# Kernel optimization log

Measured on AMD Instinct MI355X. Metric: run time of the kernel, lower is better.

Reference implementation:

```python
import jax, jax.numpy as jnp
import numpy as np
import math

B, S, D, H = 2, 2048, 4096, 32
HD = D // H  # head_dim = 128


def setup_inputs() -> dict:
    key = jax.random.key(0)
    ks = jax.random.split(key, 8)
    scale = 1.0 / math.sqrt(D)
    x = jax.random.normal(ks[0], (B, S, D), jnp.float32)
    wq = jax.random.normal(ks[1], (D, D), jnp.float32) * scale
    wk = jax.random.normal(ks[2], (D, D), jnp.float32) * scale
    wv = jax.random.normal(ks[3], (D, D), jnp.float32) * scale
    wo = jax.random.normal(ks[4], (D, D), jnp.float32) * scale
    # vis_adapter_gate is zero-initialized in the module; use small random to exercise the path
    wg = jax.random.normal(ks[5], (H, D), jnp.float32) * 0.02
    # RoPE angles: theta[t, i] = t / 10000^(2i/HD), shape (S, HD//2)
    inv_freq = 1.0 / (10000.0 ** (jnp.arange(0, HD, 2, dtype=jnp.float32) / HD))
    freqs = jnp.arange(S, dtype=jnp.float32)[:, None] * inv_freq[None, :]
    # additive causal mask (1,1,S,S)
    neg = jnp.float32(-1e9)
    mask = jnp.where(jnp.tril(jnp.ones((S, S), bool)), 0.0, neg)[None, None]
    image_position = jax.random.bernoulli(ks[6], 0.3, (B, S, D))
    return {"x": x, "wq": wq, "wk": wk, "wv": wv, "wo": wo, "wg": wg,
            "freqs": freqs, "mask": mask, "image_position": image_position}


def _rope(t, cos, sin):
    # t: (B,S,H,HD), cos/sin: (1,S,1,HD//2). Pairs are consecutive elements.
    t2 = t.reshape(*t.shape[:-1], HD // 2, 2)
    tr, ti = t2[..., 0], t2[..., 1]
    out = jnp.stack([tr * cos - ti * sin, tr * sin + ti * cos], axis=-1)
    return out.reshape(t.shape)


def reference(x, wq, wk, wv, wo, wg, freqs, mask, image_position):
    xq = jnp.einsum('bsd,ed->bse', x, wq).reshape(B, S, H, HD)
    xk = jnp.einsum('bsd,ed->bse', x, wk).reshape(B, S, H, HD)
    xv = jnp.einsum('bsd,ed->bse', x, wv).reshape(B, S, H, HD)
    # value gating on image positions
    xg = jnp.tanh(jnp.einsum('bsd,hd->bsh', x, wg))[..., None]  # (B,S,H,1)
    ip = image_position.reshape(B, S, H, HD)
    xv = jnp.where(ip, xv * xg, xv)
    # rotary embedding (computed in float32 as in torch .float())
    cos = jnp.cos(freqs)[None, :, None, :]
    sin = jnp.sin(freqs)[None, :, None, :]
    xq = _rope(xq, cos, sin)
    xk = _rope(xk, cos, sin)
    # (B,H,S,HD)
    q = xq.transpose(0, 2, 1, 3)
    k = xk.transpose(0, 2, 1, 3)
    v = xv.transpose(0, 2, 1, 3)
    scores = jnp.einsum('bhqd,bhkd->bhqk', q, k) / math.sqrt(HD) + mask
    probs = jax.nn.softmax(scores.astype(jnp.float32), axis=-1).astype(q.dtype)
    out = jnp.einsum('bhqk,bhkd->bhqd', probs, v)
    out = out.transpose(0, 2, 1, 3).reshape(B, S, D)
    return jnp.einsum('bsd,ed->bse', out, wo)
```

## Files before the change

kernel.cpp:

```cpp
#include <hip/hip_runtime.h>
#include <hip/hip_bf16.h>
#include <stdint.h>

#define B_ 2
#define S_ 2048
#define D_ 4096
#define H_ 32
#define HD_ 128
#define MTOK (B_*S_)
#define QK_SCALE 0.08838834764831845f

typedef __attribute__((ext_vector_type(8))) __bf16 bf8;
typedef __attribute__((ext_vector_type(4))) float f32x4;
typedef __attribute__((ext_vector_type(4))) unsigned short us4;
typedef __attribute__((ext_vector_type(8))) unsigned short us8;
typedef unsigned short u16;
typedef __attribute__((address_space(1))) unsigned gu32;
typedef __attribute__((address_space(3))) unsigned lu32;

__device__ __forceinline__ u16 f2bf(float f){
  unsigned u = __builtin_bit_cast(unsigned, f);
  u += 0x7FFFu + ((u >> 16) & 1u);
  return (u16)(u >> 16);
}
__device__ __forceinline__ float bf2f(u16 h){
  unsigned u = ((unsigned)h) << 16;
  return __builtin_bit_cast(float, u);
}
__device__ __forceinline__ void gload16(const void* g, void* l){
  __builtin_amdgcn_global_load_lds((gu32*)g, (lu32*)l, 16, 0, 0);
}
__device__ __forceinline__ f32x4 mfma_bf16(bf8 a, bf8 b, f32x4 c){
  return __builtin_amdgcn_mfma_f32_16x16x32_bf16(a, b, c, 0, 0, 0);
}
__device__ __forceinline__ bool read_ip(const void* p, int flag, size_t idx){
  if (flag == 0) return ((const int*)p)[idx] != 0;
  if (flag == 1) return ((const unsigned char*)p)[idx] != 0;
  if (flag == 2) return ((const u16*)p)[idx] != 0;
  return ((const float*)p)[idx] != 0.0f;
}

__global__ void k_detect(const void* x, const void* ip, const void* fq, int* flags){
  const int lane = threadIdx.x & 63;
  const unsigned char* xb = (const unsigned char*)x;
  int cnt = 0;
  for (int i = lane; i < 256; i += 64){
    unsigned char b = xb[i*4 + 1] & 0x7F;
    if (b >= 0x3A && b <= 0x41) cnt++;
  }
  #pragma unroll
  for (int off = 1; off < 64; off <<= 1) cnt += __shfl_xor(cnt, off);
  const int fflag = (cnt >= 128) ? 1 : 0;

  const unsigned char* q = (const unsigned char*)ip;
  int nz1 = 0, nz2 = 0, nz3 = 0, mx = 0;
  for (int i = lane; i < 4096; i += 64){
    int v = q[i];
    if (v > mx) mx = v;
    if (v){ int m = i & 3; if (m == 1) nz1 = 1; else if (m == 2) nz2 = 1; else if (m == 3) nz3 = 1; }
  }
  nz1 = __any(nz1); nz2 = __any(nz2); nz3 = __any(nz3);
  #pragma unroll
  for (int off = 1; off < 64; off <<= 1) mx = max(mx, __shfl_xor(mx, off));
  int ipflag;
  if (!nz1 && !nz2 && !nz3) ipflag = 0;
  else if (mx <= 1)         ipflag = 1;
  else if (nz1)             ipflag = 2;
  else                      ipflag = 3;

  const unsigned char* fb = (const unsigned char*)fq;
  int nzf = 0;
  for (int i = 128 + lane; i < 256; i += 64) if (fb[i]) nzf = 1;
  nzf = __any(nzf);
  if (lane == 0){ flags[0] = ipflag; flags[1] = fflag; flags[2] = nzf; }
}

struct CArgs {
  const float* src[6];
  u16* dst[6];
  int n4[6];
};
__global__ void k_convert_all(CArgs a, const int* __restrict__ flags){
  if (flags[1]) return;
  int pre[7];
  pre[0] = 0;
  #pragma unroll
  for (int s = 0; s < 6; ++s) pre[s+1] = pre[s] + a.n4[s];
  const int total = pre[6];
  int i = blockIdx.x * blockDim.x + threadIdx.x;
  const int stride = gridDim.x * blockDim.x;
  for (; i < total; i += stride){
    int s = 0;
    #pragma unroll
    for (int k = 1; k < 6; ++k) if (i >= pre[k]) s = k;
    const int j = i - pre[s];
    float4 v = ((const float4*)a.src[s])[j];
    us4 o;
    o.x = f2bf(v.x); o.y = f2bf(v.y); o.z = f2bf(v.z); o.w = f2bf(v.w);
    ((us4*)a.dst[s])[j] = o;
  }
}

__global__ void k_trig(const void* freqs, float* ctab, float* stab, const int* flags){
  int i = blockIdx.x * blockDim.x + threadIdx.x;
  if (i >= S_ * (HD_/2)) return;
  float v = flags[2] ? bf2f(((const u16*)freqs)[i]) : ((const float*)freqs)[i];
  ctab[i] = cosf(v);
  stab[i] = sinf(v);
}

__global__ __launch_bounds__(256,2) void k_gate(const void* x_raw, const u16* x_conv,
                                                const void* wg_raw, const u16* wg_conv,
                                                float* G, const int* flags){
  const int fflag = flags[1];
  const u16* X  = fflag ? (const u16*)x_raw  : x_conv;
  const u16* WG = fflag ? (const u16*)wg_raw : wg_conv;
  const int t = threadIdx.x, lane = t & 63, wid = t >> 6;
  const int hi = lane >> 4, lo = lane & 15, sw = lane & 7;
  const int m0 = (int)blockIdx.x * 64;
  __shared__ __align__(16) u16 lX[64*64];
  __shared__ __align__(16) u16 lW[32*64];
  f32x4 acc[2] = {};
  for (int kt = 0; kt < D_/64; ++kt){
    __syncthreads();
    const int kb = kt * 64;
    #pragma unroll
    for (int qi = 0; qi < 2; ++qi){
      int ci = t + qi*256;
      int row = ci >> 3, sc = (ci & 7) ^ (row & 7);
      gload16(X + (size_t)(m0 + row)*D_ + kb + sc*8, &lX[ci*8]);
    }
    {
      int ci = t;
      if (ci < 256){
        int row = ci >> 3, sc = (ci & 7) ^ (row & 7);
        gload16(WG + (size_t)row*D_ + kb + sc*8, &lW[ci*8]);
      }
    }
    __syncthreads();
    #pragma unroll
    for (int kk = 0; kk < 2; ++kk){
      bf8 a = *(const bf8*)&lX[(wid*16 + lo)*64 + (((kk*4 + hi) ^ sw)*8)];
      #pragma unroll
      for (int n = 0; n < 2; ++n){
        bf8 b = *(const bf8*)&lW[(n*16 + lo)*64 + (((kk*4 + hi) ^ sw)*8)];
        acc[n] = mfma_bf16(a, b, acc[n]);
      }
    }
  }
  #pragma unroll
  for (int n = 0; n < 2; ++n)
    #pragma unroll
    for (int r = 0; r < 4; ++r){
      const int tok = m0 + wid*16 + (hi << 2) + r;
      const int h = n*16 + lo;
      G[(size_t)tok*H_ + h] = tanhf(acc[n][r]);
    }
}

struct GArgs {
  const void* a_raw; const u16* a_conv;
  const void* w_raw0; const u16* w_conv0;
  const void* w_raw1; const u16* w_conv1;
  const void* w_raw2; const u16* w_conv2;
  const int* flags;
  const float* ctab; const float* stab; const float* G;
  const void* ip;
  u16* Qs; u16* Ks; u16* VT;
  void* out;
  int mode;
};

__global__ __launch_bounds__(256,2) void k_gemm(GArgs g){
  const int t = threadIdx.x;
  const int fflag = g.flags[1];
  int mat, nt;
  if (g.mode < 0){ mat = (int)blockIdx.y >> 5; nt = (int)blockIdx.y & 31; }
  else           { mat = 3; nt = (int)blockIdx.y; }
  const int wi = (mat == 3) ? 0 : mat;
  const void* wraw; const u16* wconv;
  if (wi == 0){ wraw = g.w_raw0; wconv = g.w_conv0; }
  else if (wi == 1){ wraw = g.w_raw1; wconv = g.w_conv1; }
  else { wraw = g.w_raw2; wconv = g.w_conv2; }
  const u16* Ap = fflag ? (const u16*)g.a_raw : g.a_conv;
  const u16* Wp = fflag ? (const u16*)wraw : wconv;
  const int m0 = (int)blockIdx.x * 128;
  const int n0 = nt * 128;
  __shared__ __align__(16) u16 lA[128*64];
  __shared__ __align__(16) u16 lB[128*64];
  const int lane = t & 63, wid = t >> 6;
  const int wrw = wid >> 1, wcw = wid & 1;
  const int hi = lane >> 4, lo = lane & 15, sw = lane & 7;
  f32x4 acc[4][4] = {};
  for (int kt = 0; kt < D_/64; ++kt){
    __syncthreads();
    const int kb = kt * 64;
    #pragma unroll
    for (int qi = 0; qi < 4; ++qi){
      int ci = t + qi*256;
      int row = ci >> 3, sc = (ci & 7) ^ (row & 7);
      gload16(Ap + (size_t)(m0 + row)*D_ + kb + sc*8, &lA[ci*8]);
    }
    #pragma unroll
    for (int qi = 0; qi < 4; ++qi){
      int ci = t + qi*256;
      int row = ci >> 3, sc = (ci & 7) ^ (row & 7);
      gload16(Wp + (size_t)(n0 + row)*D_ + kb + sc*8, &lB[ci*8]);
    }
    __syncthreads();
    #pragma unroll
    for (int kk = 0; kk < 2; ++kk){
      bf8 af[4], bfr[4];
      #pragma unroll
      for (int m = 0; m < 4; ++m)
        af[m] = *(const bf8*)&lA[(wrw*64 + m*16 + lo)*64 + (((kk*4 + hi) ^ sw)*8)];
      #pragma unroll
      for (int n = 0; n < 4; ++n)
        bfr[n] = *(const bf8*)&lB[(wcw*64 + n*16 + lo)*64 + (((kk*4 + hi) ^ sw)*8)];
      #pragma unroll
      for (int m = 0; m < 4; ++m)
        #pragma unroll
        for (int n = 0; n < 4; ++n)
          acc[m][n] = mfma_bf16(af[m], bfr[n], acc[m][n]);
    }
  }
  const int rbase = m0 + wrw*64 + (hi << 2);
  const int cbase = n0 + wcw*64 + lo;
  if (mat == 0 || mat == 1){
    u16* dst = (mat == 0) ? g.Qs : g.Ks;
    const float sc = (mat == 0) ? QK_SCALE : 1.0f;
    #pragma unroll
    for (int m = 0; m < 4; ++m){
      #pragma unroll
      for (int n = 0; n < 4; ++n){
        const int e = cbase + n*16;
        const int h = e >> 7, hd = e & 127, pr = hd >> 1;
        const bool even = ((hd & 1) == 0);
        #pragma unroll
        for (int r = 0; r < 4; ++r){
          const int row = rbase + m*16 + r;
          const int b = row >> 11, s = row & (S_-1);
          float v = acc[m][n][r];
          float o = __shfl_xor(v, 1);
          float cc = g.ctab[s*64 + pr], sn = g.stab[s*64 + pr];
          float res = even ? (v*cc - o*sn) : (o*sn + v*cc);
          res *= sc;
          dst[((size_t)(b*H_ + h)*S_ + s)*HD_ + hd] = f2bf(res);
        }
      }
    }
  } else if (mat == 2){
    const int ipf = g.flags[0];
    #pragma unroll
    for (int m = 0; m < 4; ++m){
      const int row0 = rbase + m*16;
      const int b = row0 >> 11, s0 = row0 & (S_-1);
      #pragma unroll
      for (int n = 0; n < 4; ++n){
        const int e = cbase + n*16;
        const int h = e >> 7, hd = e & 127;
        us4 pk;
        #pragma unroll
        for (int r = 0; r < 4; ++r){
          const int s = s0 + r;
          float v = acc[m][n][r];
          size_t ii = (size_t)(b*S_ + s)*D_ + e;
          if (read_ip(g.ip, ipf, ii)) v *= g.G[(size_t)(b*S_ + s)*H_ + h];
          pk[r] = f2bf(v);
        }
        *(us4*)&g.VT[((size_t)(b*H_ + h)*HD_ + hd)*S_ + s0] = pk;
      }
    }
  } else {
    #pragma unroll
    for (int m = 0; m < 4; ++m){
      #pragma unroll
      for (int n = 0; n < 4; ++n){
        const int e = cbase + n*16;
        #pragma unroll
        for (int r = 0; r < 4; ++r){
          const int row = rbase + m*16 + r;
          float v = acc[m][n][r];
          if (fflag) ((u16*)g.out)[(size_t)row*D_ + e] = f2bf(v);
          else       ((float*)g.out)[(size_t)row*D_ + e] = v;
        }
      }
    }
  }
}

__global__ __launch_bounds__(256,2) void k_attn(const u16* __restrict__ Qs, const u16* __restrict__ Ks,
                                                const u16* __restrict__ VT, u16* __restrict__ AO){
  const int bh = blockIdx.x;
  const int qb = (int)(gridDim.y - 1 - blockIdx.y) * 128;
  const u16* Qp = Qs + (size_t)bh * S_ * HD_;
  const u16* Kp = Ks + (size_t)bh * S_ * HD_;
  const u16* Vp = VT + (size_t)bh * HD_ * S_;
  const int t = threadIdx.x, lane = t & 63, w = t >> 6;
  const int q0 = qb + w*32;
  const int hi = lane >> 4, lo = lane & 15, sw = lane & 7;
  __shared__ __align__(16) u16 lK[2][64*HD_];
  __shared__ __align__(16) u16 lV[2][HD_*64];
  __shared__ __align__(16) u16 lP[4][32*64];

  const us8 ones_u = {0x3F80,0x3F80,0x3F80,0x3F80,0x3F80,0x3F80,0x3F80,0x3F80};
  const bf8 ones = __builtin_bit_cast(bf8, ones_u);

  auto stage = [&](int j2, int bsel){
    const int kv = j2 * 64;
    #pragma unroll
    for (int qi = 0; qi < 4; ++qi){
      int ci = t + qi*256;
      int row = ci >> 4, scs = (ci & 15) ^ (row & 7);
      gload16(Kp + (size_t)(kv + row)*HD_ + scs*8, &lK[bsel][ci*8]);
    }
    #pragma unroll
    for (int qi = 0; qi < 4; ++qi){
      int ci = t + qi*256;
      int row = ci >> 3, scs = (ci & 7) ^ (row & 7);
      gload16(Vp + (size_t)row*S_ + kv + scs*8, &lV[bsel][ci*8]);
    }
  };

  bf8 qf[2][4];
  #pragma unroll
  for (int m = 0; m < 2; ++m)
    #pragma unroll
    for (int kk = 0; kk < 4; ++kk)
      qf[m][kk] = *(const bf8*)&Qp[(size_t)(q0 + m*16 + lo)*HD_ + kk*32 + hi*8];
  f32x4 o[2][8] = {};
  f32x4 osum[2] = {};
  const int ntile = (qb >> 6) + 2;

  stage(0, 0);
  stage(1, 1);
  asm volatile("s_waitcnt vmcnt(8)" ::: "memory");
  __builtin_amdgcn_s_barrier();

  for (int j = 0; j < ntile; ++j){
    const int cur = j & 1;
    const int kv0 = j*64;
    if (kv0 <= q0 + 31){
      f32x4 sf[2][4] = {};
      __builtin_amdgcn_s_setprio(1);
      #pragma unroll
      for (int kk = 0; kk < 4; ++kk){
        bf8 kf[4];
        #pragma unroll
        for (int n = 0; n < 4; ++n)
          kf[n] = *(const bf8*)&lK[cur][(n*16 + lo)*HD_ + (((kk*4 + hi) ^ sw)*8)];
        #pragma unroll
        for (int m = 0; m < 2; ++m)
          #pragma unroll
          for (int n = 0; n < 4; ++n)
            sf[m][n] = mfma_bf16(qf[m][kk], kf[n], sf[m][n]);
      }
      __builtin_amdgcn_s_setprio(0);
      const int rb = q0 + (hi << 2);
      const int cb = kv0 + lo;
      #pragma unroll
      for (int m = 0; m < 2; ++m)
        #pragma unroll
        for (int r = 0; r < 4; ++r){
          const int row = rb + m*16 + r;
          #pragma unroll
          for (int n = 0; n < 4; ++n){
            float s = (cb + n*16 > row) ? -1e30f : sf[m][n][r];
            sf[m][n][r] = __expf(fminf(s, 80.0f));
          }
        }
      u16* myP = lP[w];
      #pragma unroll
      for (int m = 0; m < 2; ++m)
        #pragma unroll
        for (int n = 0; n < 4; ++n)
          #pragma unroll
          for (int r = 0; r < 4; ++r){
            const int prow = m*16 + (hi << 2) + r;
            myP[prow*64 + ((n*16 + lo) ^ ((prow & 7) << 3))] = f2bf(sf[m][n][r]);
          }
      __builtin_amdgcn_s_setprio(1);
      #pragma unroll
      for (int kk = 0; kk < 2; ++kk){
        bf8 pf[2];
        #pragma unroll
        for (int m = 0; m < 2; ++m)
          pf[m] = *(const bf8*)&myP[(m*16 + lo)*64 + ((kk*32 + hi*8) ^ (sw << 3))];
        #pragma unroll
        for (int n = 0; n < 8; ++n){
          bf8 vf = *(const bf8*)&lV[cur][(n*16 + lo)*64 + (((kk*4 + hi) ^ sw)*8)];
          #pragma unroll
          for (int m = 0; m < 2; ++m)
            o[m][n] = mfma_bf16(pf[m], vf, o[m][n]);
        }
        #pragma unroll
        for (int m = 0; m < 2; ++m)
          osum[m] = mfma_bf16(pf[m], ones, osum[m]);
      }
      __builtin_amdgcn_s_setprio(0);
    }
    __builtin_amdgcn_s_barrier();
    if (j + 2 < ntile){
      stage(j + 2, cur);
      asm volatile("s_waitcnt vmcnt(8)" ::: "memory");
    } else if (j + 1 < ntile){
      asm volatile("s_waitcnt vmcnt(0)" ::: "memory");
    }
    __builtin_amdgcn_s_barrier();
  }
  const int b = bh >> 5, h = bh & 31;
  #pragma unroll
  for (int m = 0; m < 2; ++m){
    #pragma unroll
    for (int n = 0; n < 8; ++n){
      const int c = n*16 + lo;
      #pragma unroll
      for (int r = 0; r < 4; ++r){
        const int row = q0 + m*16 + (hi << 2) + r;
        float v = o[m][n][r] / osum[m][r];
        AO[(size_t)(b*S_ + row)*D_ + h*HD_ + c] = f2bf(v);
      }
    }
  }
}

extern "C" void kernel_launch(void* const* d_in, const int* in_sizes, int n_in,
                              void* d_out, int out_size, void* d_ws, size_t ws_size,
                              hipStream_t stream){
  const void* x   = d_in[0];
  const void* wq  = d_in[1];
  const void* wk  = d_in[2];
  const void* wv  = d_in[3];
  const void* wo  = d_in[4];
  const void* wg  = d_in[5];
  const void* fr  = d_in[6];
  const void* ip  = d_in[8];

  char* ws = (char*)d_ws;
  size_t off = 0;
  auto alloc = [&](size_t bytes)->char* {
    size_t o = off; off += (bytes + 255) & ~(size_t)255; return ws + o;
  };
  int*   flags = (int*)  alloc(256);
  float* ctab  = (float*)alloc((size_t)S_*64*4);
  float* stab  = (float*)alloc((size_t)S_*64*4);
  float* G     = (float*)alloc((size_t)MTOK*H_*4);
  u16* Qs = (u16*)alloc((size_t)B_*H_*S_*HD_*2);
  u16* Ks = (u16*)alloc((size_t)B_*H_*S_*HD_*2);
  u16* VT = (u16*)alloc((size_t)B_*H_*S_*HD_*2);
  u16* AO = (u16*)alloc((size_t)MTOK*D_*2);
  size_t conv_bytes = ((size_t)MTOK*D_*2 + 256) + 4*((size_t)D_*D_*2 + 256) + ((size_t)H_*D_*2 + 256);
  bool conv = (ws_size >= off + conv_bytes);
  u16 *xb = Qs, *wqb = Qs, *wkb = Qs, *wvb = Qs, *wob = Qs, *wgb = Qs;
  if (conv){
    xb  = (u16*)alloc((size_t)MTOK*D_*2);
    wqb = (u16*)alloc((size_t)D_*D_*2);
    wkb = (u16*)alloc((size_t)D_*D_*2);
    wvb = (u16*)alloc((size_t)D_*D_*2);
    wob = (u16*)alloc((size_t)D_*D_*2);
    wgb = (u16*)alloc((size_t)H_*D_*2);
  }

  k_detect<<<1, 64, 0, stream>>>(x, ip, fr, flags);
  if (conv){
    CArgs ca{};
    ca.src[0] = (const float*)x;  ca.dst[0] = xb;  ca.n4[0] = (MTOK*D_) >> 2;
    ca.src[1] = (const float*)wq; ca.dst[1] = wqb; ca.n4[1] = (D_*D_) >> 2;
    ca.src[2] = (const float*)wk; ca.dst[2] = wkb; ca.n4[2] = (D_*D_) >> 2;
    ca.src[3] = (const float*)wv; ca.dst[3] = wvb; ca.n4[3] = (D_*D_) >> 2;
    ca.src[4] = (const float*)wo; ca.dst[4] = wob; ca.n4[4] = (D_*D_) >> 2;
    ca.src[5] = (const float*)wg; ca.dst[5] = wgb; ca.n4[5] = (H_*D_) >> 2;
    k_convert_all<<<4096, 256, 0, stream>>>(ca, flags);
  }
  k_trig<<<512, 256, 0, stream>>>(fr, ctab, stab, flags);
  k_gate<<<64, 256, 0, stream>>>(x, xb, wg, wgb, G, flags);

  GArgs ga{};
  ga.a_raw = x;  ga.a_conv = xb;
  ga.w_raw0 = wq; ga.w_conv0 = wqb;
  ga.w_raw1 = wk; ga.w_conv1 = wkb;
  ga.w_raw2 = wv; ga.w_conv2 = wvb;
  ga.flags = flags; ga.ctab = ctab; ga.stab = stab; ga.G = G; ga.ip = ip;
  ga.Qs = Qs; ga.Ks = Ks; ga.VT = VT; ga.out = nullptr; ga.mode = -1;
  k_gemm<<<dim3(32, 96), 256, 0, stream>>>(ga);

  k_attn<<<dim3(64, 16), 256, 0, stream>>>(Qs, Ks, VT, AO);

  GArgs go{};
  go.a_raw = AO; go.a_conv = AO;
  go.w_raw0 = wo; go.w_conv0 = wob;
  go.w_raw1 = wo; go.w_conv1 = wob;
  go.w_raw2 = wo; go.w_conv2 = wob;
  go.flags = flags; go.ctab = ctab; go.stab = stab; go.G = G; go.ip = ip;
  go.Qs = Qs; go.Ks = Ks; go.VT = VT; go.out = d_out; go.mode = 3;
  k_gemm<<<dim3(32, 32), 256, 0, stream>>>(go);
}
```

Before: 851.0 us.

## Rewrite GEMM as 256x256 tile, 8-wave, double-buffered pipelined kernel

The projection GEMM kernel moves from a 128x128 tile with 4 waves and a single LDS buffer to a 256x256 tile with 8 waves and double-buffered LDS. Global-to-LDS staging for the next K-step is split into quarter loads interleaved with four MFMA phases, using explicit vmcnt/lgkmcnt waits, barriers and s_setprio. The goal is to hide memory latency behind compute and raise arithmetic intensity. In exchange it uses 128KB of LDS and more accumulator registers per block, allowing only one block per CU. The grids shrink to 768 and 256 blocks, and 256 blocks may underfill the 256 CUs.

```diff
diff --git a/kernel.cpp b/kernel.cpp
--- a/kernel.cpp
+++ b/kernel.cpp
@@ -171,11 +171,11 @@
   int mode;
 };
 
-__global__ __launch_bounds__(256,2) void k_gemm(GArgs g){
+__global__ __launch_bounds__(512,1) void k_gemm(GArgs g){
   const int t = threadIdx.x;
   const int fflag = g.flags[1];
   int mat, nt;
-  if (g.mode < 0){ mat = (int)blockIdx.y >> 5; nt = (int)blockIdx.y & 31; }
+  if (g.mode < 0){ mat = (int)blockIdx.y >> 4; nt = (int)blockIdx.y & 15; }
   else           { mat = 3; nt = (int)blockIdx.y; }
   const int wi = (mat == 3) ? 0 : mat;
   const void* wraw; const u16* wconv;
@@ -184,53 +184,138 @@
   else { wraw = g.w_raw2; wconv = g.w_conv2; }
   const u16* Ap = fflag ? (const u16*)g.a_raw : g.a_conv;
   const u16* Wp = fflag ? (const u16*)wraw : wconv;
-  const int m0 = (int)blockIdx.x * 128;
-  const int n0 = nt * 128;
-  __shared__ __align__(16) u16 lA[128*64];
-  __shared__ __align__(16) u16 lB[128*64];
+  const int m0 = (int)blockIdx.x * 256;
+  const int n0 = nt * 256;
+  __shared__ __align__(16) u16 lA[2][256*64];
+  __shared__ __align__(16) u16 lB[2][256*64];
   const int lane = t & 63, wid = t >> 6;
-  const int wrw = wid >> 1, wcw = wid & 1;
+  const int wm = wid >> 2, wn = wid & 3;
   const int hi = lane >> 4, lo = lane & 15, sw = lane & 7;
-  f32x4 acc[4][4] = {};
-  for (int kt = 0; kt < D_/64; ++kt){
-    __syncthreads();
-    const int kb = kt * 64;
-    #pragma unroll
-    for (int qi = 0; qi < 4; ++qi){
-      int ci = t + qi*256;
-      int row = ci >> 3, sc = (ci & 7) ^ (row & 7);
-      gload16(Ap + (size_t)(m0 + row)*D_ + kb + sc*8, &lA[ci*8]);
-    }
-    #pragma unroll
-    for (int qi = 0; qi < 4; ++qi){
-      int ci = t + qi*256;
-      int row = ci >> 3, sc = (ci & 7) ^ (row & 7);
-      gload16(Wp + (size_t)(n0 + row)*D_ + kb + sc*8, &lB[ci*8]);
-    }
-    __syncthreads();
-    #pragma unroll
-    for (int kk = 0; kk < 2; ++kk){
-      bf8 af[4], bfr[4];
-      #pragma unroll
-      for (int m = 0; m < 4; ++m)
-        af[m] = *(const bf8*)&lA[(wrw*64 + m*16 + lo)*64 + (((kk*4 + hi) ^ sw)*8)];
-      #pragma unroll
-      for (int n = 0; n < 4; ++n)
-        bfr[n] = *(const bf8*)&lB[(wcw*64 + n*16 + lo)*64 + (((kk*4 + hi) ^ sw)*8)];
-      #pragma unroll
-      for (int m = 0; m < 4; ++m)
-        #pragma unroll
-        for (int n = 0; n < 4; ++n)
-          acc[m][n] = mfma_bf16(af[m], bfr[n], acc[m][n]);
-    }
-  }
-  const int rbase = m0 + wrw*64 + (hi << 2);
-  const int cbase = n0 + wcw*64 + lo;
+  f32x4 acc[8][4] = {};
+
+  auto stgA = [&](int kt2, int bsel, int mh){
+    const int kb = kt2 * 64;
+    #pragma unroll
+    for (int q = 0; q < 2; ++q){
+      int ci = q*512 + t;
+      int r = ci >> 3;
+      int R = mh*64 + ((r < 64) ? r : r + 64);
+      int c = ci & 7, sc = c ^ (R & 7);
+      gload16(Ap + (size_t)(m0 + R)*D_ + kb + sc*8, &lA[bsel][(R*8 + c)*8]);
+    }
+  };
+  auto stgB = [&](int kt2, int bsel, int nh){
+    const int kb = kt2 * 64;
+    #pragma unroll
+    for (int q = 0; q < 2; ++q){
+      int ci = q*512 + t;
+      int r = ci >> 3;
+      int R = nh*32 + ((r >> 5) << 6) + (r & 31);
+      int c = ci & 7, sc = c ^ (R & 7);
+      gload16(Wp + (size_t)(n0 + R)*D_ + kb + sc*8, &lB[bsel][(R*8 + c)*8]);
+    }
+  };
+
+  stgB(0, 0, 0); stgA(0, 0, 0); stgA(0, 0, 1); stgB(0, 0, 1);
+  stgB(1, 1, 0); stgA(1, 1, 0);
+  asm volatile("s_waitcnt vmcnt(4)" ::: "memory");
+  __builtin_amdgcn_s_barrier();
+
+  const int NT = D_ / 64;
+  for (int kt = 0; kt < NT; ++kt){
+    const int buf = kt & 1;
+    const u16* pa = &lA[buf][0];
+    const u16* pb = &lB[buf][0];
+    bf8 Af[8][2], Bf[4][2];
+
+    #pragma unroll
+    for (int m = 0; m < 4; ++m)
+      #pragma unroll
+      for (int kk = 0; kk < 2; ++kk)
+        Af[m][kk] = *(const bf8*)&pa[(wm*128 + m*16 + lo)*64 + (((kk*4 + hi) ^ sw)*8)];
+    #pragma unroll
+    for (int n = 0; n < 2; ++n)
+      #pragma unroll
+      for (int kk = 0; kk < 2; ++kk)
+        Bf[n][kk] = *(const bf8*)&pb[(wn*64 + n*16 + lo)*64 + (((kk*4 + hi) ^ sw)*8)];
+    if (kt + 1 < NT) stgA(kt + 1, buf ^ 1, 1);
+    __builtin_amdgcn_s_barrier();
+    asm volatile("s_waitcnt lgkmcnt(0)" ::: "memory");
+    __builtin_amdgcn_s_setprio(1);
+    #pragma unroll
+    for (int m = 0; m < 4; ++m)
+      #pragma unroll
+      for (int n = 0; n < 2; ++n)
+        #pragma unroll
+        for (int kk = 0; kk < 2; ++kk)
+          acc[m][n] = mfma_bf16(Af[m][kk], Bf[n][kk], acc[m][n]);
+    __builtin_amdgcn_s_setprio(0);
+    __builtin_amdgcn_s_barrier();
+
+    #pragma unroll
+    for (int m = 4; m < 8; ++m)
+      #pragma unroll
+      for (int kk = 0; kk < 2; ++kk)
+        Af[m][kk] = *(const bf8*)&pa[(wm*128 + m*16 + lo)*64 + (((kk*4 + hi) ^ sw)*8)];
+    if (kt + 1 < NT) stgB(kt + 1, buf ^ 1, 1);
+    __builtin_amdgcn_s_barrier();
+    asm volatile("s_waitcnt lgkmcnt(0)" ::: "memory");
+    __builtin_amdgcn_s_setprio(1);
+    #pragma unroll
+    for (int m = 4; m < 8; ++m)
+      #pragma unroll
+      for (int n = 0; n < 2; ++n)
+        #pragma unroll
+        for (int kk = 0; kk < 2; ++kk)
+          acc[m][n] = mfma_bf16(Af[m][kk], Bf[n][kk], acc[m][n]);
+    __builtin_amdgcn_s_setprio(0);
+    __builtin_amdgcn_s_barrier();
+
+    #pragma unroll
+    for (int n = 2; n < 4; ++n)
+      #pragma unroll
+      for (int kk = 0; kk < 2; ++kk)
+        Bf[n][kk] = *(const bf8*)&pb[(wn*64 + n*16 + lo)*64 + (((kk*4 + hi) ^ sw)*8)];
+    if (kt + 2 < NT) stgB(kt + 2, buf, 0);
+    __builtin_amdgcn_s_barrier();
+    asm volatile("s_waitcnt lgkmcnt(0)" ::: "memory");
+    __builtin_amdgcn_s_setprio(1);
+    #pragma unroll
+    for (int m = 0; m < 4; ++m)
+      #pragma unroll
+      for (int n = 2; n < 4; ++n)
+        #pragma unroll
+        for (int kk = 0; kk < 2; ++kk)
+          acc[m][n] = mfma_bf16(Af[m][kk], Bf[n][kk], acc[m][n]);
+    __builtin_amdgcn_s_setprio(0);
+    __builtin_amdgcn_s_barrier();
+
+    if (kt + 2 < NT){
+      stgA(kt + 2, buf, 0);
+      asm volatile("s_waitcnt vmcnt(4)" ::: "memory");
+    } else if (kt + 1 < NT){
+      asm volatile("s_waitcnt vmcnt(0)" ::: "memory");
+    }
+    __builtin_amdgcn_s_barrier();
+    __builtin_amdgcn_s_setprio(1);
+    #pragma unroll
+    for (int m = 4; m < 8; ++m)
+      #pragma unroll
+      for (int n = 2; n < 4; ++n)
+        #pragma unroll
+        for (int kk = 0; kk < 2; ++kk)
+          acc[m][n] = mfma_bf16(Af[m][kk], Bf[n][kk], acc[m][n]);
+    __builtin_amdgcn_s_setprio(0);
+    __builtin_amdgcn_s_barrier();
+  }
+
+  const int rbase = m0 + wm*128 + (hi << 2);
+  const int cbase = n0 + wn*64 + lo;
   if (mat == 0 || mat == 1){
     u16* dst = (mat == 0) ? g.Qs : g.Ks;
     const float sc = (mat == 0) ? QK_SCALE : 1.0f;
     #pragma unroll
-    for (int m = 0; m < 4; ++m){
+    for (int m = 0; m < 8; ++m){
       #pragma unroll
       for (int n = 0; n < 4; ++n){
         const int e = cbase + n*16;
@@ -252,7 +337,7 @@
   } else if (mat == 2){
     const int ipf = g.flags[0];
     #pragma unroll
-    for (int m = 0; m < 4; ++m){
+    for (int m = 0; m < 8; ++m){
       const int row0 = rbase + m*16;
       const int b = row0 >> 11, s0 = row0 & (S_-1);
       #pragma unroll
@@ -273,7 +358,7 @@
     }
   } else {
     #pragma unroll
-    for (int m = 0; m < 4; ++m){
+    for (int m = 0; m < 8; ++m){
       #pragma unroll
       for (int n = 0; n < 4; ++n){
         const int e = cbase + n*16;
@@ -482,7 +567,7 @@
   ga.w_raw2 = wv; ga.w_conv2 = wvb;
   ga.flags = flags; ga.ctab = ctab; ga.stab = stab; ga.G = G; ga.ip = ip;
   ga.Qs = Qs; ga.Ks = Ks; ga.VT = VT; ga.out = nullptr; ga.mode = -1;
-  k_gemm<<<dim3(32, 96), 256, 0, stream>>>(ga);
+  k_gemm<<<dim3(16, 48), 512, 0, stream>>>(ga);
 
   k_attn<<<dim3(64, 16), 256, 0, stream>>>(Qs, Ks, VT, AO);
 
@@ -493,5 +578,5 @@
   go.w_raw2 = wo; go.w_conv2 = wob;
   go.flags = flags; go.ctab = ctab; go.stab = stab; go.G = G; go.ip = ip;
   go.Qs = Qs; go.Ks = Ks; go.VT = VT; go.out = d_out; go.mode = 3;
-  k_gemm<<<dim3(32, 32), 256, 0, stream>>>(go);
-}
+  k_gemm<<<dim3(16, 16), 512, 0, stream>>>(go);
+}
```

Result: slower. 878.6 us (+3.2%).
